# Kernel tuning notes

Measured on AMD Instinct MI355X. Metric: run time of the kernel, lower is better.

Reference implementation:

```python
import jax, jax.numpy as jnp
import numpy as np

L, H, K, N_IN, B = 8, 512, 16, 512, 8192  # layers, nodes/layer, fan-in, input nodes, batch


def setup_inputs() -> dict:
    key = jax.random.key(0)
    k_x, k_w, k_b = jax.random.split(key, 3)
    x = jax.random.normal(k_x, (B, N_IN), dtype=jnp.float32)
    # DAG links: node in layer l may read any of the N_IN + l*H previously computed nodes
    rng = np.random.default_rng(0)
    link_idx = np.stack(
        [rng.integers(0, N_IN + l * H, size=(H, K)) for l in range(L)]
    ).astype(np.int32)  # [L, H, K]
    weights = jax.random.normal(k_w, (L, H, K), dtype=jnp.float32) * 0.3
    bias = jax.random.normal(k_b, (L, H), dtype=jnp.float32) * 0.1
    return {"x": x, "link_idx": jnp.asarray(link_idx), "weights": weights, "bias": bias}


def reference(x, link_idx, weights, bias):
    # values dict -> growing [B, n_nodes_so_far] buffer; per-node Linear(K,1)+Sigmoid
    values = x  # [B, N_IN]
    for l in range(L):  # small fixed structural loop over topological layers
        g = values[:, link_idx[l]]                      # gather predecessor values [B, H, K]
        out = jax.nn.sigmoid(
            jnp.einsum("bhk,hk->bh", g, weights[l]) + bias[l]
        )                                               # [B, H]
        values = jnp.concatenate([values, out], axis=1)
    return values[:, -H:]  # output nodes = last layer
```

## Files before the change

### kernel.cpp

```cpp
#include <hip/hip_runtime.h>
#include <hip/hip_fp16.h>

#define LAYERS 8
#define H      512
#define K      16
#define N_IN   512
#define BATCH  8192
#define R      8
#define NT     512
#define LDS_COLS 4096
#define PARAM_N  (LAYERS * H * K)


__global__ __launch_bounds__(512)
void ffn_prep_kernel(const int*   __restrict__ link_idx,
                     const float* __restrict__ weights,
                     int*         __restrict__ idx2,
                     float*       __restrict__ w2)
{
    const int t    = blockIdx.x * 512 + threadIdx.x;
    const int base = t * K;

    int idx[K]; float w[K];
    #pragma unroll
    for (int k = 0; k < K; ++k) { idx[k] = link_idx[base + k]; w[k] = weights[base + k]; }

    int cnt[8];
    #pragma unroll
    for (int p = 0; p < 8; ++p) cnt[p] = 0;
    #pragma unroll
    for (int k = 0; k < K; ++k) cnt[idx[k] & 7]++;
    int ofs[8]; int s = 0;
    #pragma unroll
    for (int p = 0; p < 8; ++p) { ofs[p] = s; s += cnt[p]; }
    int sid[K]; float sw[K];
    #pragma unroll
    for (int k = 0; k < K; ++k) {
        const int p = idx[k] & 7;
        const int d = ofs[p]++;
        sid[d] = idx[k]; sw[d] = w[k];
    }

    const int rot = t & 15;
    #pragma unroll
    for (int j = 0; j < K; ++j) {
        const int srcslot = (j + rot) & 15;
        idx2[base + j] = sid[srcslot] << 4;
        w2[base + j]  = sw[srcslot];
    }
}

template <int PRESCALED>
__global__ __launch_bounds__(NT, 2)
void ffn_fused_kernel(const float* __restrict__ x,
                      const int*   __restrict__ idxp,
                      const float* __restrict__ wp,
                      const float* __restrict__ bias,
                      float*       __restrict__ out)
{
    __shared__ __align__(16) __half vals[LDS_COLS * R];

    const int tid  = threadIdx.x;
    const int row0 = blockIdx.x * R;

    {
        const int c = tid;
        float v[R];
        #pragma unroll
        for (int r = 0; r < R; ++r)
            v[r] = x[(row0 + r) * N_IN + c];
        __half2 p[R / 2];
        #pragma unroll
        for (int r = 0; r < R / 2; ++r)
            p[r] = __floats2half2_rn(v[2 * r], v[2 * r + 1]);
        *(uint4*)&vals[c * R] = *(const uint4*)p;
    }

    int   idxA[K]; float wA[K]; float bA;
    {
        const int base = tid * K;
        #pragma unroll
        for (int q = 0; q < 4; ++q) {
            *(int4*)  &idxA[4 * q] = ((const int4*)  (idxp + base))[q];
            *(float4*)&wA  [4 * q] = ((const float4*)(wp   + base))[q];
        }
        if (!PRESCALED) {
            #pragma unroll
            for (int k = 0; k < K; ++k) idxA[k] <<= 4;
        }
        bA = bias[tid];
    }

    __syncthreads();

    #pragma unroll
    for (int l = 0; l < LAYERS; ++l) {
        int idxB[K]; float wB[K]; float bB = 0.0f;
        if (l < LAYERS - 1) {
            const int nb = ((l + 1) * H + tid) * K;
            #pragma unroll
            for (int q = 0; q < 4; ++q) {
                *(int4*)  &idxB[4 * q] = ((const int4*)  (idxp + nb))[q];
                *(float4*)&wB  [4 * q] = ((const float4*)(wp   + nb))[q];
            }
            if (!PRESCALED) {
                #pragma unroll
                for (int k = 0; k < K; ++k) idxB[k] <<= 4;
            }
            bB = bias[(l + 1) * H + tid];
        }

        float acc[R];
        #pragma unroll
        for (int r = 0; r < R; ++r) acc[r] = bA;

        #pragma unroll
        for (int k = 0; k < K; ++k) {
            const uint4 g = *(const uint4*)((const char*)vals + idxA[k]);
            const __half2* hp = (const __half2*)&g;
            const float wk = wA[k];
            #pragma unroll
            for (int r = 0; r < R / 2; ++r) {
                const float2 f = __half22float2(hp[r]);
                acc[2 * r]     = fmaf(f.x, wk, acc[2 * r]);
                acc[2 * r + 1] = fmaf(f.y, wk, acc[2 * r + 1]);
            }
        }

        #pragma unroll
        for (int r = 0; r < R; ++r)
            acc[r] = __builtin_amdgcn_rcpf(1.0f + __expf(-acc[r]));

        if (l < LAYERS - 1) {
            __half2 p[R / 2];
            #pragma unroll
            for (int r = 0; r < R / 2; ++r)
                p[r] = __floats2half2_rn(acc[2 * r], acc[2 * r + 1]);
            *(uint4*)&vals[(N_IN + l * H + tid) * R] = *(const uint4*)p;
            __syncthreads();
            #pragma unroll
            for (int k = 0; k < K; ++k) { idxA[k] = idxB[k]; wA[k] = wB[k]; }
            bA = bB;
        } else {
            #pragma unroll
            for (int r = 0; r < R; ++r)
                out[(row0 + r) * H + tid] = acc[r];
        }
    }
}

extern "C" void kernel_launch(void* const* d_in, const int* in_sizes, int n_in,
                              void* d_out, int out_size, void* d_ws, size_t ws_size,
                              hipStream_t stream) {
    const float* x        = (const float*)d_in[0];
    const int*   link_idx = (const int*)  d_in[1];
    const float* weights  = (const float*)d_in[2];
    const float* bias     = (const float*)d_in[3];
    float*       out      = (float*)d_out;

    const size_t need = 2 * (size_t)PARAM_N * 4;

    if (d_ws != nullptr && ws_size >= need) {
        int*   idx2 = (int*)d_ws;
        float* w2   = (float*)((char*)d_ws + PARAM_N * sizeof(int));
        ffn_prep_kernel<<<dim3(LAYERS), dim3(512), 0, stream>>>(link_idx, weights, idx2, w2);
        ffn_fused_kernel<1><<<dim3(BATCH / R), dim3(NT), 0, stream>>>(x, idx2, w2, bias, out);
    } else {
        ffn_fused_kernel<0><<<dim3(BATCH / R), dim3(NT), 0, stream>>>(x, link_idx, weights, bias, out);
    }
}
```

Measured before the change: 118.6 us.

## Schedule per-wave gather order to balance LDS bank slots per k-step

Result: slower. 170.0 us (+43.3%).

```diff
diff --git a/kernel.cpp b/kernel.cpp
--- a/kernel.cpp
+++ b/kernel.cpp
@@ -10,43 +10,56 @@
 #define NT     512
 #define LDS_COLS 4096
 #define PARAM_N  (LAYERS * H * K)
+#define SLOTS  8
 
 
-__global__ __launch_bounds__(512)
-void ffn_prep_kernel(const int*   __restrict__ link_idx,
-                     const float* __restrict__ weights,
-                     int*         __restrict__ idx2,
-                     float*       __restrict__ w2)
+__global__ __launch_bounds__(64)
+void ffn_sched_kernel(const int*   __restrict__ link_idx,
+                      const float* __restrict__ weights,
+                      int*         __restrict__ idx2,
+                      float*       __restrict__ w2)
 {
-    const int t    = blockIdx.x * 512 + threadIdx.x;
-    const int base = t * K;
+    __shared__ int cnt[SLOTS];
+    const int lane    = threadIdx.x;
+    const int wavepos = blockIdx.x & 7;
+    const int layer   = blockIdx.x >> 3;
+    const int t       = wavepos * 64 + lane;
+    const int base    = (layer * H + t) * K;
 
-    int idx[K]; float w[K];
-    #pragma unroll
-    for (int k = 0; k < K; ++k) { idx[k] = link_idx[base + k]; w[k] = weights[base + k]; }
-
-    int cnt[8];
-    #pragma unroll
-    for (int p = 0; p < 8; ++p) cnt[p] = 0;
-    #pragma unroll
-    for (int k = 0; k < K; ++k) cnt[idx[k] & 7]++;
-    int ofs[8]; int s = 0;
-    #pragma unroll
-    for (int p = 0; p < 8; ++p) { ofs[p] = s; s += cnt[p]; }
-    int sid[K]; float sw[K];
+    int idx[K]; float w[K]; int slot[K];
     #pragma unroll
     for (int k = 0; k < K; ++k) {
-        const int p = idx[k] & 7;
-        const int d = ofs[p]++;
-        sid[d] = idx[k]; sw[d] = w[k];
+        idx[k]  = link_idx[base + k];
+        w[k]    = weights[base + k];
+        slot[k] = idx[k] & (SLOTS - 1);
     }
 
-    const int rot = t & 15;
-    #pragma unroll
+    unsigned rem = 0xFFFFu;
     for (int j = 0; j < K; ++j) {
-        const int srcslot = (j + rot) & 15;
-        idx2[base + j] = sid[srcslot] << 4;
-        w2[base + j]  = sw[srcslot];
+        if (lane < SLOTS) cnt[lane] = 0;
+        __syncthreads();
+        int chosen = -1;
+        for (int iter = 0; iter < 10; ++iter) {
+            if (__all(chosen >= 0)) break;
+            const int cap = (iter < 8) ? (8 + iter) : (1 << 30);
+            if (chosen < 0) {
+                int best_e = 0, best_load = 1 << 30;
+                #pragma unroll
+                for (int e = 0; e < K; ++e) {
+                    if (rem & (1u << e)) {
+                        const int ld = cnt[slot[e]];
+                        if (ld < best_load) { best_load = ld; best_e = e; }
+                    }
+                }
+                const int old = atomicAdd(&cnt[slot[best_e]], 1);
+                if (old < cap) { chosen = best_e; rem &= ~(1u << best_e); }
+                else            atomicAdd(&cnt[slot[best_e]], -1);
+            }
+            __syncthreads();
+        }
+        idx2[base + j] = idx[chosen] << 4;
+        w2 [base + j] = w[chosen];
+        __syncthreads();
     }
 }
 
@@ -163,7 +176,7 @@
     if (d_ws != nullptr && ws_size >= need) {
         int*   idx2 = (int*)d_ws;
         float* w2   = (float*)((char*)d_ws + PARAM_N * sizeof(int));
-        ffn_prep_kernel<<<dim3(LAYERS), dim3(512), 0, stream>>>(link_idx, weights, idx2, w2);
+        ffn_sched_kernel<<<dim3(64), dim3(64), 0, stream>>>(link_idx, weights, idx2, w2);
         ffn_fused_kernel<1><<<dim3(BATCH / R), dim3(NT), 0, stream>>>(x, idx2, w2, bias, out);
     } else {
         ffn_fused_kernel<0><<<dim3(BATCH / R), dim3(NT), 0, stream>>>(x, link_idx, weights, bias, out);
```
